# Optimization experiments

Hardware: AMD Instinct MI355X
Metric: run time of the kernel (lower is better)

Reference implementation:

```python
import jax, jax.numpy as jnp
import numpy as np

BATCH = 16384
IN_F = 4096
OUT_F = 4096
CP_H = 4
CP_W = 4
CP_B = 4


def _cubic_interp_matrix(n_out: int, n_cp: int, a: float = -0.75) -> jnp.ndarray:
    """Dense (n_out, n_cp) matrix replicating torch bicubic interpolation
    (Keys cubic convolution, a=-0.75) along one axis with align_corners=True
    and border replication (index clamping)."""
    # source coordinate for each output index (align_corners=True)
    x = jnp.arange(n_out, dtype=jnp.float32) * ((n_cp - 1) / (n_out - 1))
    x0 = jnp.floor(x)
    t = x - x0                      # fractional offset in [0,1)
    x0i = x0.astype(jnp.int32)

    def cub_inner(s):   # |s| <= 1
        return ((a + 2.0) * s - (a + 3.0)) * s * s + 1.0

    def cub_outer(s):   # 1 < |s| < 2
        return ((a * s - 5.0 * a) * s + 8.0 * a) * s - 4.0 * a

    # weights for taps at offsets -1, 0, +1, +2
    ws = (cub_outer(t + 1.0), cub_inner(t), cub_inner(1.0 - t), cub_outer(2.0 - t))
    A = jnp.zeros((n_out, n_cp), dtype=jnp.float32)
    for k, w in enumerate(ws):
        idx = jnp.clip(x0i + (k - 1), 0, n_cp - 1)  # replicate border
        A = A + w[:, None] * jax.nn.one_hot(idx, n_cp, dtype=jnp.float32)
    return A


def _linear_interp_matrix(n_out: int, n_cp: int) -> jnp.ndarray:
    """Dense (n_out, n_cp) matrix replicating torch 1-D linear interpolation
    with align_corners=True."""
    x = jnp.arange(n_out, dtype=jnp.float32) * ((n_cp - 1) / (n_out - 1))
    lo = jnp.floor(x).astype(jnp.int32)
    t = x - lo.astype(jnp.float32)
    hi = jnp.clip(lo + 1, 0, n_cp - 1)
    oh = lambda i: jax.nn.one_hot(i, n_cp, dtype=jnp.float32)
    return (1.0 - t)[:, None] * oh(lo) + t[:, None] * oh(hi)


def setup_inputs() -> dict:
    key = jax.random.key(0)
    k1, k2, k3 = jax.random.split(key, 3)
    return {
        "x": jax.random.normal(k1, (BATCH, IN_F), dtype=jnp.float32),
        "weight_cp": jax.random.normal(k2, (CP_H, CP_W), dtype=jnp.float32) * 0.02,
        "bias_cp": jax.random.normal(k3, (CP_B,), dtype=jnp.float32) * 0.02,
    }


def reference(x, weight_cp, bias_cp):
    # Bicubic-interpolated dense weight: W = A_out @ CP @ A_in^T  (out, in)
    A_out = _cubic_interp_matrix(OUT_F, CP_H)
    A_in = _cubic_interp_matrix(IN_F, CP_W)
    W = A_out @ weight_cp @ A_in.T
    # Linearly interpolated bias (out,)
    bias = _linear_interp_matrix(OUT_F, CP_B) @ bias_cp
    # F.linear: y = x @ W^T + b
    return x @ W.T + bias
```

## Files before the change

kernel.cpp:

```cpp
#include <hip/hip_runtime.h>
#include <cstddef>

#define BATCH 16384
#define IN_F  4096
#define OUT_F 4096
#define ROWS_PER_BLOCK 64

__device__ __forceinline__ float cub_inner(float s) {
    return (1.25f * s - 2.25f) * s * s + 1.0f;
}
__device__ __forceinline__ float cub_outer(float s) {
    return ((-0.75f * s + 3.75f) * s - 6.0f) * s + 3.0f;
}

__device__ __forceinline__ void cubic_row(int i, float& a0, float& a1, float& a2, float& a3) {
    const float inv = 3.0f / 4095.0f;
    const float xi = (float)i * inv;
    const float x0 = floorf(xi);
    const float t  = xi - x0;
    const int   c  = (int)x0;
    const float w0 = cub_outer(t + 1.0f);
    const float w1 = cub_inner(t);
    const float w2 = cub_inner(1.0f - t);
    const float w3 = cub_outer(2.0f - t);
    if (c == 0)      { a0 = w0 + w1; a1 = w2;   a2 = w3;   a3 = 0.0f; }
    else if (c == 1) { a0 = w0;      a1 = w1;   a2 = w2;   a3 = w3; }
    else if (c == 2) { a0 = 0.0f;    a1 = w0;   a2 = w1;   a3 = w2 + w3; }
    else             { a0 = 0.0f;    a1 = 0.0f; a2 = w0;   a3 = w1 + w2 + w3; }
}

__global__ __launch_bounds__(256) void k_project(const float* __restrict__ x,
                                                 float* __restrict__ tproj) {
    const int b   = blockIdx.x;
    const int tid = threadIdx.x;
    const float4* xrow = (const float4*)(x + (size_t)b * IN_F);
    float acc0 = 0.f, acc1 = 0.f, acc2 = 0.f, acc3 = 0.f;
#pragma unroll
    for (int k = 0; k < 4; ++k) {
        const int v4 = k * 256 + tid;
        const float4 xv = xrow[v4];
        const int i = v4 * 4;
        float a0, a1, a2, a3;
        cubic_row(i + 0, a0, a1, a2, a3);
        acc0 += a0 * xv.x; acc1 += a1 * xv.x; acc2 += a2 * xv.x; acc3 += a3 * xv.x;
        cubic_row(i + 1, a0, a1, a2, a3);
        acc0 += a0 * xv.y; acc1 += a1 * xv.y; acc2 += a2 * xv.y; acc3 += a3 * xv.y;
        cubic_row(i + 2, a0, a1, a2, a3);
        acc0 += a0 * xv.z; acc1 += a1 * xv.z; acc2 += a2 * xv.z; acc3 += a3 * xv.z;
        cubic_row(i + 3, a0, a1, a2, a3);
        acc0 += a0 * xv.w; acc1 += a1 * xv.w; acc2 += a2 * xv.w; acc3 += a3 * xv.w;
    }
#pragma unroll
    for (int off = 32; off > 0; off >>= 1) {
        acc0 += __shfl_down(acc0, off);
        acc1 += __shfl_down(acc1, off);
        acc2 += __shfl_down(acc2, off);
        acc3 += __shfl_down(acc3, off);
    }
    __shared__ float lds[4][4];
    const int wid = tid >> 6;
    if ((tid & 63) == 0) {
        lds[wid][0] = acc0; lds[wid][1] = acc1; lds[wid][2] = acc2; lds[wid][3] = acc3;
    }
    __syncthreads();
    if (tid < 4) {
        tproj[(size_t)b * 4 + tid] = lds[0][tid] + lds[1][tid] + lds[2][tid] + lds[3][tid];
    }
}

__global__ __launch_bounds__(256) void k_expand(const float* __restrict__ tproj,
                                                const float* __restrict__ cp,
                                                const float* __restrict__ bcp,
                                                float* __restrict__ y) {
    const int oq = blockIdx.x * 256 + threadIdx.x;
    const int o0 = oq * 4;
    float cpr[16];
#pragma unroll
    for (int k = 0; k < 16; ++k) cpr[k] = cp[k];
    const float b0 = bcp[0], b1 = bcp[1], b2 = bcp[2], b3 = bcp[3];

    float we[4][4];
    float bs[4];
#pragma unroll
    for (int j = 0; j < 4; ++j) {
        const int o = o0 + j;
        float h0, h1, h2, h3;
        cubic_row(o, h0, h1, h2, h3);
#pragma unroll
        for (int w = 0; w < 4; ++w)
            we[j][w] = h0 * cpr[w] + h1 * cpr[4 + w] + h2 * cpr[8 + w] + h3 * cpr[12 + w];
        const float xb = (float)o * (3.0f / 4095.0f);
        const float lo = floorf(xb);
        const float tb = xb - lo;
        const int   l  = (int)lo;
        const float blo = (l == 0) ? b0 : (l == 1) ? b1 : (l == 2) ? b2 : b3;
        const float bhi = (l >= 2) ? b3 : (l == 1) ? b2 : b1;
        bs[j] = (1.0f - tb) * blo + tb * bhi;
    }

    const int r0 = blockIdx.y * ROWS_PER_BLOCK;
#pragma unroll 4
    for (int r = 0; r < ROWS_PER_BLOCK; ++r) {
        const int b = r0 + r;
        const float4 tv = *(const float4*)(tproj + (size_t)b * 4);
        float4 out;
        out.x = bs[0] + we[0][0]*tv.x + we[0][1]*tv.y + we[0][2]*tv.z + we[0][3]*tv.w;
        out.y = bs[1] + we[1][0]*tv.x + we[1][1]*tv.y + we[1][2]*tv.z + we[1][3]*tv.w;
        out.z = bs[2] + we[2][0]*tv.x + we[2][1]*tv.y + we[2][2]*tv.z + we[2][3]*tv.w;
        out.w = bs[3] + we[3][0]*tv.x + we[3][1]*tv.y + we[3][2]*tv.z + we[3][3]*tv.w;
        *(float4*)(y + (size_t)b * OUT_F + o0) = out;
    }
}

extern "C" void kernel_launch(void* const* d_in, const int* in_sizes, int n_in,
                              void* d_out, int out_size, void* d_ws, size_t ws_size,
                              hipStream_t stream) {
    const float* x   = (const float*)d_in[0];
    const float* cp  = (const float*)d_in[1];
    const float* bcp = (const float*)d_in[2];
    float* y = (float*)d_out;
    float* tproj = (float*)d_ws;

    k_project<<<dim3(BATCH), dim3(256), 0, stream>>>(x, tproj);
    dim3 g2(OUT_F / (256 * 4), BATCH / ROWS_PER_BLOCK);
    k_expand<<<g2, dim3(256), 0, stream>>>(tproj, cp, bcp, y);
}
```

Before: 487.5 us.

## Precompute interpolation tables once and reuse them across rows in projection

A new init kernel precomputes the input cubic-weight table, the expanded output weight table (A_out·CP) and the bias table into workspace. The projection kernel loads these weights once per thread, processes 8 rows per block, and writes per-wave partial sums without an LDS barrier. The expand kernel reads the precomputed tables, reduces the partials into shared memory, and uses 32 rows per block. This removes repeated per-element cubic weight evaluation, at the cost of an extra launch and extra workspace traffic.

```diff
diff --git a/kernel.cpp b/kernel.cpp
--- a/kernel.cpp
+++ b/kernel.cpp
@@ -4,7 +4,11 @@
 #define BATCH 16384
 #define IN_F  4096
 #define OUT_F 4096
-#define ROWS_PER_BLOCK 64
+
+#define WS_PARTIAL_OFF 0
+#define WS_AIN_OFF     (1u << 20)
+#define WS_E_OFF       (WS_AIN_OFF + (64u << 10))
+#define WS_BIAS_OFF    (WS_E_OFF + (64u << 10))
 
 __device__ __forceinline__ float cub_inner(float s) {
     return (1.25f * s - 2.25f) * s * s + 1.0f;
@@ -29,86 +33,122 @@
     else             { a0 = 0.0f;    a1 = 0.0f; a2 = w0;   a3 = w1 + w2 + w3; }
 }
 
+__global__ __launch_bounds__(256) void k_init(const float* __restrict__ cp,
+                                              const float* __restrict__ bcp,
+                                              float* __restrict__ ws) {
+    const int i = blockIdx.x * 256 + threadIdx.x;
+    float a0, a1, a2, a3;
+    cubic_row(i, a0, a1, a2, a3);
+
+    float4* ain  = (float4*)((char*)ws + WS_AIN_OFF);
+    float4* etab = (float4*)((char*)ws + WS_E_OFF);
+    float*  btab = (float*)((char*)ws + WS_BIAS_OFF);
+
+    ain[i] = make_float4(a0, a1, a2, a3);
+
+    float4 e;
+    e.x = a0 * cp[0]  + a1 * cp[4]  + a2 * cp[8]  + a3 * cp[12];
+    e.y = a0 * cp[1]  + a1 * cp[5]  + a2 * cp[9]  + a3 * cp[13];
+    e.z = a0 * cp[2]  + a1 * cp[6]  + a2 * cp[10] + a3 * cp[14];
+    e.w = a0 * cp[3]  + a1 * cp[7]  + a2 * cp[11] + a3 * cp[15];
+    etab[i] = e;
+
+    const float xb = (float)i * (3.0f / 4095.0f);
+    const float lo = floorf(xb);
+    const float tb = xb - lo;
+    const int   l  = (int)lo;
+    const float blo = bcp[l < 3 ? l : 3];
+    const float bhi = bcp[(l + 1) < 3 ? (l + 1) : 3];
+    btab[i] = (1.0f - tb) * blo + tb * bhi;
+}
+
 __global__ __launch_bounds__(256) void k_project(const float* __restrict__ x,
-                                                 float* __restrict__ tproj) {
-    const int b   = blockIdx.x;
-    const int tid = threadIdx.x;
-    const float4* xrow = (const float4*)(x + (size_t)b * IN_F);
-    float acc0 = 0.f, acc1 = 0.f, acc2 = 0.f, acc3 = 0.f;
+                                                 float* __restrict__ ws) {
+    const int tid  = threadIdx.x;
+    const int w    = tid >> 6;
+    const int lane = tid & 63;
+    const int r0   = blockIdx.x * 8;
+
+    const float4* ain = (const float4*)((char*)ws + WS_AIN_OFF);
+    float4* partial   = (float4*)((char*)ws + WS_PARTIAL_OFF);
+
+    int c4[4];
+    float4 wq[4][4];
 #pragma unroll
-    for (int k = 0; k < 4; ++k) {
-        const int v4 = k * 256 + tid;
-        const float4 xv = xrow[v4];
-        const int i = v4 * 4;
-        float a0, a1, a2, a3;
-        cubic_row(i + 0, a0, a1, a2, a3);
-        acc0 += a0 * xv.x; acc1 += a1 * xv.x; acc2 += a2 * xv.x; acc3 += a3 * xv.x;
-        cubic_row(i + 1, a0, a1, a2, a3);
-        acc0 += a0 * xv.y; acc1 += a1 * xv.y; acc2 += a2 * xv.y; acc3 += a3 * xv.y;
-        cubic_row(i + 2, a0, a1, a2, a3);
-        acc0 += a0 * xv.z; acc1 += a1 * xv.z; acc2 += a2 * xv.z; acc3 += a3 * xv.z;
-        cubic_row(i + 3, a0, a1, a2, a3);
-        acc0 += a0 * xv.w; acc1 += a1 * xv.w; acc2 += a2 * xv.w; acc3 += a3 * xv.w;
+    for (int g = 0; g < 4; ++g) {
+        c4[g] = 256 * w + 64 * g + lane;
+#pragma unroll
+        for (int e = 0; e < 4; ++e)
+            wq[g][e] = ain[4 * c4[g] + e];
     }
+
+    for (int r = 0; r < 8; ++r) {
+        const int row = r0 + r;
+        const float4* xr = (const float4*)(x + (size_t)row * IN_F);
+        float acc0 = 0.f, acc1 = 0.f, acc2 = 0.f, acc3 = 0.f;
 #pragma unroll
-    for (int off = 32; off > 0; off >>= 1) {
-        acc0 += __shfl_down(acc0, off);
-        acc1 += __shfl_down(acc1, off);
-        acc2 += __shfl_down(acc2, off);
-        acc3 += __shfl_down(acc3, off);
-    }
-    __shared__ float lds[4][4];
-    const int wid = tid >> 6;
-    if ((tid & 63) == 0) {
-        lds[wid][0] = acc0; lds[wid][1] = acc1; lds[wid][2] = acc2; lds[wid][3] = acc3;
-    }
-    __syncthreads();
-    if (tid < 4) {
-        tproj[(size_t)b * 4 + tid] = lds[0][tid] + lds[1][tid] + lds[2][tid] + lds[3][tid];
+        for (int g = 0; g < 4; ++g) {
+            const float4 xv = xr[c4[g]];
+            acc0 += wq[g][0].x * xv.x; acc1 += wq[g][0].y * xv.x;
+            acc2 += wq[g][0].z * xv.x; acc3 += wq[g][0].w * xv.x;
+            acc0 += wq[g][1].x * xv.y; acc1 += wq[g][1].y * xv.y;
+            acc2 += wq[g][1].z * xv.y; acc3 += wq[g][1].w * xv.y;
+            acc0 += wq[g][2].x * xv.z; acc1 += wq[g][2].y * xv.z;
+            acc2 += wq[g][2].z * xv.z; acc3 += wq[g][2].w * xv.z;
+            acc0 += wq[g][3].x * xv.w; acc1 += wq[g][3].y * xv.w;
+            acc2 += wq[g][3].z * xv.w; acc3 += wq[g][3].w * xv.w;
+        }
+#pragma unroll
+        for (int m = 32; m > 0; m >>= 1) {
+            acc0 += __shfl_xor(acc0, m);
+            acc1 += __shfl_xor(acc1, m);
+            acc2 += __shfl_xor(acc2, m);
+            acc3 += __shfl_xor(acc3, m);
+        }
+        if (lane == 0)
+            partial[row * 4 + w] = make_float4(acc0, acc1, acc2, acc3);
     }
 }
 
-__global__ __launch_bounds__(256) void k_expand(const float* __restrict__ tproj,
-                                                const float* __restrict__ cp,
-                                                const float* __restrict__ bcp,
+__global__ __launch_bounds__(256) void k_expand(const float* __restrict__ ws,
                                                 float* __restrict__ y) {
-    const int oq = blockIdx.x * 256 + threadIdx.x;
-    const int o0 = oq * 4;
-    float cpr[16];
-#pragma unroll
-    for (int k = 0; k < 16; ++k) cpr[k] = cp[k];
-    const float b0 = bcp[0], b1 = bcp[1], b2 = bcp[2], b3 = bcp[3];
+    const int tid = threadIdx.x;
+    const int oq  = blockIdx.x * 256 + tid;
+    const int o0  = oq * 4;
+    const int r0  = blockIdx.y * 32;
 
-    float we[4][4];
-    float bs[4];
-#pragma unroll
-    for (int j = 0; j < 4; ++j) {
-        const int o = o0 + j;
-        float h0, h1, h2, h3;
-        cubic_row(o, h0, h1, h2, h3);
-#pragma unroll
-        for (int w = 0; w < 4; ++w)
-            we[j][w] = h0 * cpr[w] + h1 * cpr[4 + w] + h2 * cpr[8 + w] + h3 * cpr[12 + w];
-        const float xb = (float)o * (3.0f / 4095.0f);
-        const float lo = floorf(xb);
-        const float tb = xb - lo;
-        const int   l  = (int)lo;
-        const float blo = (l == 0) ? b0 : (l == 1) ? b1 : (l == 2) ? b2 : b3;
-        const float bhi = (l >= 2) ? b3 : (l == 1) ? b2 : b1;
-        bs[j] = (1.0f - tb) * blo + tb * bhi;
+    const float4* partial = (const float4*)((const char*)ws + WS_PARTIAL_OFF);
+    const float4* etab    = (const float4*)((const char*)ws + WS_E_OFF);
+    const float4* btab    = (const float4*)((const char*)ws + WS_BIAS_OFF);
+
+    float4 ew0 = etab[o0 + 0];
+    float4 ew1 = etab[o0 + 1];
+    float4 ew2 = etab[o0 + 2];
+    float4 ew3 = etab[o0 + 3];
+    float4 bq  = btab[oq];
+
+    __shared__ float4 sp[32];
+    if (tid < 32) {
+        float4 p0 = partial[(r0 + tid) * 4 + 0];
+        float4 p1 = partial[(r0 + tid) * 4 + 1];
+        float4 p2 = partial[(r0 + tid) * 4 + 2];
+        float4 p3 = partial[(r0 + tid) * 4 + 3];
+        sp[tid] = make_float4(p0.x + p1.x + p2.x + p3.x,
+                              p0.y + p1.y + p2.y + p3.y,
+                              p0.z + p1.z + p2.z + p3.z,
+                              p0.w + p1.w + p2.w + p3.w);
     }
+    __syncthreads();
 
-    const int r0 = blockIdx.y * ROWS_PER_BLOCK;
-#pragma unroll 4
-    for (int r = 0; r < ROWS_PER_BLOCK; ++r) {
-        const int b = r0 + r;
-        const float4 tv = *(const float4*)(tproj + (size_t)b * 4);
+#pragma unroll 8
+    for (int r = 0; r < 32; ++r) {
+        const float4 tv = sp[r];
         float4 out;
-        out.x = bs[0] + we[0][0]*tv.x + we[0][1]*tv.y + we[0][2]*tv.z + we[0][3]*tv.w;
-        out.y = bs[1] + we[1][0]*tv.x + we[1][1]*tv.y + we[1][2]*tv.z + we[1][3]*tv.w;
-        out.z = bs[2] + we[2][0]*tv.x + we[2][1]*tv.y + we[2][2]*tv.z + we[2][3]*tv.w;
-        out.w = bs[3] + we[3][0]*tv.x + we[3][1]*tv.y + we[3][2]*tv.z + we[3][3]*tv.w;
-        *(float4*)(y + (size_t)b * OUT_F + o0) = out;
+        out.x = bq.x + ew0.x * tv.x + ew0.y * tv.y + ew0.z * tv.z + ew0.w * tv.w;
+        out.y = bq.y + ew1.x * tv.x + ew1.y * tv.y + ew1.z * tv.z + ew1.w * tv.w;
+        out.z = bq.z + ew2.x * tv.x + ew2.y * tv.y + ew2.z * tv.z + ew2.w * tv.w;
+        out.w = bq.w + ew3.x * tv.x + ew3.y * tv.y + ew3.z * tv.z + ew3.w * tv.w;
+        *(float4*)(y + (size_t)(r0 + r) * OUT_F + o0) = out;
     }
 }
 
@@ -118,10 +158,10 @@
     const float* x   = (const float*)d_in[0];
     const float* cp  = (const float*)d_in[1];
     const float* bcp = (const float*)d_in[2];
-    float* y = (float*)d_out;
-    float* tproj = (float*)d_ws;
+    float* y  = (float*)d_out;
+    float* ws = (float*)d_ws;
 
-    k_project<<<dim3(BATCH), dim3(256), 0, stream>>>(x, tproj);
-    dim3 g2(OUT_F / (256 * 4), BATCH / ROWS_PER_BLOCK);
-    k_expand<<<g2, dim3(256), 0, stream>>>(tproj, cp, bcp, y);
+    k_init   <<<dim3(16),        dim3(256), 0, stream>>>(cp, bcp, ws);
+    k_project<<<dim3(2048),      dim3(256), 0, stream>>>(x, ws);
+    k_expand <<<dim3(4, 512),    dim3(256), 0, stream>>>(ws, y);
 }
```

After: 491.4 us. No clear change (+0.8%).
